# Performance work log

Hardware: AMD Instinct MI355X
Metric: run time of the kernel (lower is better)

Reference implementation:

```python
import jax, jax.numpy as jnp
import numpy as np
from jax import lax

B, T, C_IN, C_OUT, HW = 4, 8, 64, 64, 96

def conv2d(x, w, b):
    # x: [B,C,H,W], w: [O,I,3,3] (OIHW), SAME padding, stride 1
    y = lax.conv_general_dilated(x, w, (1, 1), 'SAME',
                                 dimension_numbers=('NCHW', 'OIHW', 'NCHW'))
    return y + b[None, :, None, None]

def setup_inputs() -> dict:
    key = jax.random.key(0)
    ks = jax.random.split(key, 4)
    s = 1.0 / np.sqrt((C_IN + C_OUT) * 9)
    return {
        'x': jax.random.normal(ks[0], (B, T, C_IN, HW, HW), jnp.float32),
        'w_r': jax.random.normal(ks[1], (C_OUT, C_IN + C_OUT, 3, 3), jnp.float32) * s,
        'b_r': jnp.zeros((C_OUT,), jnp.float32),
        'w_z': jax.random.normal(ks[2], (C_OUT, C_IN + C_OUT, 3, 3), jnp.float32) * s,
        'b_z': jnp.zeros((C_OUT,), jnp.float32),
        'w_h': jax.random.normal(ks[3], (C_OUT, C_IN + C_OUT, 3, 3), jnp.float32) * s,
        'b_h': jnp.zeros((C_OUT,), jnp.float32),
    }

def reference(x, w_r, b_r, w_z, b_z, w_h, b_h):
    # x: [B,T,C_in,H,W] -> time-major [T,B,C_in,H,W]
    xt = jnp.transpose(x.reshape(B, T, C_IN, HW, HW), (1, 0, 2, 3, 4))
    h0 = jnp.zeros((B, C_OUT, HW, HW), x.dtype)

    def step(h, x_i):
        xh = jnp.concatenate([x_i, h], axis=1)          # [B, C_in+C_out, H, W]
        r = jax.nn.sigmoid(conv2d(xh, w_r, b_r))         # reset gate
        z = jax.nn.sigmoid(conv2d(xh, w_z, b_z))         # update gate
        h_tilde = jnp.tanh(conv2d(jnp.concatenate([x_i, r * h], axis=1), w_h, b_h))
        h_new = (1.0 - z) * h + z * h_tilde
        return h_new, h_new

    _, outs = lax.scan(step, h0, xt)                     # [T,B,C_out,H,W]
    outs = jnp.transpose(outs, (1, 0, 2, 3, 4))          # [B,T,C_out,H,W]
    return outs.reshape(-1, C_OUT, HW, HW)               # [B*T,C_out,H,W]
```

## Files before the change

kernel.cpp:

```cpp
#include <hip/hip_runtime.h>
#include <hip/hip_fp16.h>

#define HWD  96
#define NPIX (HWD*HWD)
#define CIN  64
#define COUT 64
#define CTOT 128
#define BB   4
#define TT   8
#define WSTR (CTOT*9)

typedef short bf16x8 __attribute__((ext_vector_type(8)));
typedef float f32x4  __attribute__((ext_vector_type(4)));

__device__ __forceinline__ float sigmoid_(float v){ return 1.0f/(1.0f+__expf(-v)); }
__device__ __forceinline__ float tanh_(float v){
    float e = __expf(2.0f*fabsf(v));
    float t = 1.0f - 2.0f/(e+1.0f);
    return copysignf(t, v);
}
__device__ __forceinline__ short f2bf(float f){
    unsigned u = __float_as_uint(f);
    u += 0x7fffu + ((u>>16)&1u);
    return (short)(u>>16);
}
__device__ __forceinline__ short f2h(float f){
    return (short)__half_as_ushort(__float2half(f));
}
__device__ __forceinline__ float h2f(short s){
    return __half2float(__ushort_as_half((unsigned short)s));
}

__global__ __launch_bounds__(256) void convert_x_all(const float* __restrict__ x,
                                                     short* __restrict__ xt){
    __shared__ float tile[64][65];
    const int bt  = blockIdx.y;
    const int px0 = blockIdx.x * 64;
    const float* src = x + (size_t)bt*CIN*NPIX;
    short* dst = xt + (size_t)bt*NPIX*CIN;
    const int tid = threadIdx.x;
#pragma unroll
    for (int i = 0; i < 16; ++i){
        int ic = i*4 + (tid>>6);
        int pl = tid & 63;
        tile[ic][pl] = src[(size_t)ic*NPIX + px0 + pl];
    }
    __syncthreads();
#pragma unroll
    for (int i = 0; i < 16; ++i){
        int ic = tid & 63;
        int pl = i*4 + (tid>>6);
        dst[(size_t)(px0+pl)*CIN + ic] = f2bf(tile[ic][pl]);
    }
}

__global__ __launch_bounds__(256) void convert_x(const float* __restrict__ x,
                                                 short* __restrict__ xt, int t){
    __shared__ float tile[64][65];
    const int b   = blockIdx.y;
    const int px0 = blockIdx.x * 64;
    const float* src = x + ((size_t)(b*TT + t)*CIN)*NPIX;
    short* dst = xt + ((size_t)b*NPIX)*CIN;
    const int tid = threadIdx.x;
#pragma unroll
    for (int i = 0; i < 16; ++i){
        int ic = i*4 + (tid>>6);
        int pl = tid & 63;
        tile[ic][pl] = src[(size_t)ic*NPIX + px0 + pl];
    }
    __syncthreads();
#pragma unroll
    for (int i = 0; i < 16; ++i){
        int ic = tid & 63;
        int pl = i*4 + (tid>>6);
        dst[(size_t)(px0+pl)*CIN + ic] = f2bf(tile[ic][pl]);
    }
}

__global__ __launch_bounds__(256) void convert_w(const float* __restrict__ wr,
    const float* __restrict__ wz, const float* __restrict__ wh,
    short* __restrict__ wfrag, short* __restrict__ zpad){
    const int g = blockIdx.x*256 + threadIdx.x;
    if (g < 128) zpad[g] = 0;
    const int lane = g & 63, rest = g >> 6;
    const int mt = rest & 3, kc = (rest>>2)&3, rem = rest>>4;
    const int tap = rem % 9, c = rem / 9;
    const float* wsrc = (c==0) ? wr : (c==1) ? wz : wh;
    const int oc  = mt*16 + (lane&15);
    const int ctb = kc*32 + (lane>>4)*8;
    bf16x8 v;
#pragma unroll
    for (int j=0;j<8;++j)
        v[j] = f2bf(wsrc[(size_t)oc*WSTR + (size_t)(ctb+j)*9 + tap]);
    *(bf16x8*)(wfrag + (size_t)g*8) = v;
}

__global__ __launch_bounds__(256) void precompute_ux(
    const short* __restrict__ xt, const short* __restrict__ wfrag,
    const short* __restrict__ zpad, short* __restrict__ ux)
{
    const int lane = threadIdx.x & 63;
    const int wave = threadIdx.x >> 6;
    const int quad = lane >> 4, col = lane & 15;
    const int bt = blockIdx.y, c = blockIdx.z;
    const int n_base = blockIdx.x*128 + wave*32;

    int px[2], xx[2], yy[2];
#pragma unroll
    for (int nt=0; nt<2; ++nt){
        px[nt] = n_base + nt*16 + col;
        yy[nt] = px[nt]/HWD;
        xx[nt] = px[nt] - yy[nt]*HWD;
    }

    f32x4 acc[4][2];
#pragma unroll
    for (int mt=0;mt<4;++mt)
#pragma unroll
    for (int nt=0;nt<2;++nt) acc[mt][nt] = f32x4{0.f,0.f,0.f,0.f};

    const short* xs = xt + (size_t)bt*NPIX*CIN;
    for (int tap=0; tap<9; ++tap){
        const int ky = tap/3, kx = tap-3*ky;
        const int off = (ky-1)*HWD + (kx-1);
        const short* bp[2];
#pragma unroll
        for (int nt=0;nt<2;++nt){
            bool v = ((unsigned)(yy[nt]+ky-1) < HWD) && ((unsigned)(xx[nt]+kx-1) < HWD);
            bp[nt] = v ? (xs + (size_t)(px[nt]+off)*CIN) : zpad;
        }
#pragma unroll
        for (int kcl=0; kcl<2; ++kcl){
            bf16x8 bfr[2];
#pragma unroll
            for (int nt=0;nt<2;++nt)
                bfr[nt] = *(const bf16x8*)(bp[nt] + kcl*32 + quad*8);
            const short* wc = wfrag + (size_t)(((c*9+tap)*4 + kcl)*4)*64*8;
#pragma unroll
            for (int mt=0;mt<4;++mt){
                bf16x8 a = *(const bf16x8*)(wc + (size_t)(mt*64+lane)*8);
#pragma unroll
                for (int nt=0;nt<2;++nt)
                    acc[mt][nt] = __builtin_amdgcn_mfma_f32_16x16x32_bf16(
                        a, bfr[nt], acc[mt][nt], 0, 0, 0);
            }
        }
    }

    short* uxs = ux + ((size_t)c*(BB*TT) + bt)*NPIX*COUT;
#pragma unroll
    for (int mt=0; mt<4; ++mt){
        const int ocb = mt*16 + quad*4;
#pragma unroll
        for (int nt=0; nt<2; ++nt){
            short4 v;
            v.x = f2h(acc[mt][nt][0]); v.y = f2h(acc[mt][nt][1]);
            v.z = f2h(acc[mt][nt][2]); v.w = f2h(acc[mt][nt][3]);
            *(short4*)(uxs + (size_t)px[nt]*COUT + ocb) = v;
        }
    }
}

__global__ __launch_bounds__(256) void gates2(
    const short* __restrict__ htb, const short* __restrict__ wfrag,
    const short* __restrict__ zpad, const short* __restrict__ ux,
    const float* __restrict__ br, const float* __restrict__ bz,
    float* __restrict__ out, short* __restrict__ rht, int t)
{
    const int lane = threadIdx.x & 63;
    const int wave = threadIdx.x >> 6;
    const int quad = lane >> 4, col = lane & 15;
    const int b = blockIdx.y, c = blockIdx.z;
    const int n_base = blockIdx.x*128 + wave*32;

    int px[2], xx[2], yy[2];
#pragma unroll
    for (int nt=0; nt<2; ++nt){
        px[nt] = n_base + nt*16 + col;
        yy[nt] = px[nt]/HWD;
        xx[nt] = px[nt] - yy[nt]*HWD;
    }

    const short* uxs = ux + (((size_t)c*BB + b)*TT + t)*NPIX*COUT;
    short4 uxv[4][2];
#pragma unroll
    for (int mt=0; mt<4; ++mt)
#pragma unroll
    for (int nt=0; nt<2; ++nt)
        uxv[mt][nt] = *(const short4*)(uxs + (size_t)px[nt]*COUT + mt*16 + quad*4);

    f32x4 acc[4][2];
#pragma unroll
    for (int mt=0;mt<4;++mt)
#pragma unroll
    for (int nt=0;nt<2;++nt) acc[mt][nt] = f32x4{0.f,0.f,0.f,0.f};

    if (t > 0){
        const short* hs = htb + (size_t)b*NPIX*COUT;
        for (int tap=0; tap<9; ++tap){
            const int ky = tap/3, kx = tap-3*ky;
            const int off = (ky-1)*HWD + (kx-1);
            const short* bp[2];
#pragma unroll
            for (int nt=0;nt<2;++nt){
                bool v = ((unsigned)(yy[nt]+ky-1) < HWD) && ((unsigned)(xx[nt]+kx-1) < HWD);
                bp[nt] = v ? (hs + (size_t)(px[nt]+off)*COUT) : zpad;
            }
#pragma unroll
            for (int kcl=0; kcl<2; ++kcl){
                bf16x8 bfr[2];
#pragma unroll
                for (int nt=0;nt<2;++nt)
                    bfr[nt] = *(const bf16x8*)(bp[nt] + kcl*32 + quad*8);
                const short* wc = wfrag + (size_t)(((c*9+tap)*4 + 2+kcl)*4)*64*8;
#pragma unroll
                for (int mt=0;mt<4;++mt){
                    bf16x8 a = *(const bf16x8*)(wc + (size_t)(mt*64+lane)*8);
#pragma unroll
                    for (int nt=0;nt<2;++nt)
                        acc[mt][nt] = __builtin_amdgcn_mfma_f32_16x16x32_bf16(
                            a, bfr[nt], acc[mt][nt], 0, 0, 0);
                }
            }
        }
    }

    const float* hprev = out + ((size_t)(b*TT+t-1)*COUT)*NPIX;
    if (c == 0){
        short* rhs = rht + (size_t)b*NPIX*COUT;
#pragma unroll
        for (int mt=0; mt<4; ++mt){
            const int ocb = mt*16 + quad*4;
#pragma unroll
            for (int nt=0; nt<2; ++nt){
                const int p = px[nt];
                const short* uq = (const short*)&uxv[mt][nt];
                short rh4[4];
#pragma unroll
                for (int reg=0; reg<4; ++reg){
                    const int oc = ocb + reg;
                    float r  = sigmoid_(acc[mt][nt][reg] + h2f(uq[reg]) + br[oc]);
                    float hv = (t>0) ? hprev[(size_t)oc*NPIX + p] : 0.0f;
                    rh4[reg] = f2bf(r*hv);
                }
                *(short4*)(rhs + (size_t)p*COUT + ocb) =
                    make_short4(rh4[0], rh4[1], rh4[2], rh4[3]);
            }
        }
    } else {
        float* zout = out + ((size_t)(b*TT+t)*COUT)*NPIX;
#pragma unroll
        for (int mt=0; mt<4; ++mt){
            const int ocb = mt*16 + quad*4;
#pragma unroll
            for (int nt=0; nt<2; ++nt){
                const int p = px[nt];
                const short* uq = (const short*)&uxv[mt][nt];
#pragma unroll
                for (int reg=0; reg<4; ++reg){
                    const int oc = ocb + reg;
                    zout[(size_t)oc*NPIX + p] =
                        sigmoid_(acc[mt][nt][reg] + h2f(uq[reg]) + bz[oc]);
                }
            }
        }
    }
}

__global__ __launch_bounds__(256) void cand2(
    const short* __restrict__ rht, const short* __restrict__ wfrag,
    const short* __restrict__ zpad, const short* __restrict__ ux,
    const float* __restrict__ bh, float* __restrict__ out,
    short* __restrict__ htb, int t)
{
    const int lane = threadIdx.x & 63;
    const int wave = threadIdx.x >> 6;
    const int quad = lane >> 4, col = lane & 15;
    const int b = blockIdx.y, mh = blockIdx.z;
    const int n_base = blockIdx.x*128 + wave*32;

    int px[2], xx[2], yy[2];
#pragma unroll
    for (int nt=0; nt<2; ++nt){
        px[nt] = n_base + nt*16 + col;
        yy[nt] = px[nt]/HWD;
        xx[nt] = px[nt] - yy[nt]*HWD;
    }

    const short* uxs = ux + (((size_t)2*BB + b)*TT + t)*NPIX*COUT;
    short4 uxv[2][2];
#pragma unroll
    for (int mtl=0; mtl<2; ++mtl)
#pragma unroll
    for (int nt=0; nt<2; ++nt)
        uxv[mtl][nt] = *(const short4*)(uxs + (size_t)px[nt]*COUT + (mh*2+mtl)*16 + quad*4);

    f32x4 acc[2][2];
#pragma unroll
    for (int mtl=0;mtl<2;++mtl)
#pragma unroll
    for (int nt=0;nt<2;++nt) acc[mtl][nt] = f32x4{0.f,0.f,0.f,0.f};

    if (t > 0){
        const short* rs = rht + (size_t)b*NPIX*COUT;
        for (int tap=0; tap<9; ++tap){
            const int ky = tap/3, kx = tap-3*ky;
            const int off = (ky-1)*HWD + (kx-1);
            const short* bp[2];
#pragma unroll
            for (int nt=0;nt<2;++nt){
                bool v = ((unsigned)(yy[nt]+ky-1) < HWD) && ((unsigned)(xx[nt]+kx-1) < HWD);
                bp[nt] = v ? (rs + (size_t)(px[nt]+off)*COUT) : zpad;
            }
#pragma unroll
            for (int kcl=0; kcl<2; ++kcl){
                bf16x8 bfr[2];
#pragma unroll
                for (int nt=0;nt<2;++nt)
                    bfr[nt] = *(const bf16x8*)(bp[nt] + kcl*32 + quad*8);
                const short* wc = wfrag + (size_t)(((2*9+tap)*4 + 2+kcl)*4)*64*8;
#pragma unroll
                for (int mtl=0;mtl<2;++mtl){
                    const int mt = mh*2 + mtl;
                    bf16x8 a = *(const bf16x8*)(wc + (size_t)(mt*64+lane)*8);
#pragma unroll
                    for (int nt=0;nt<2;++nt)
                        acc[mtl][nt] = __builtin_amdgcn_mfma_f32_16x16x32_bf16(
                            a, bfr[nt], acc[mtl][nt], 0, 0, 0);
                }
            }
        }
    }

    float* o = out + ((size_t)(b*TT+t)*COUT)*NPIX;
    const float* hprev = out + ((size_t)(b*TT+t-1)*COUT)*NPIX;
    short* hts = htb + (size_t)b*NPIX*COUT;
#pragma unroll
    for (int mtl=0; mtl<2; ++mtl){
        const int ocb = (mh*2+mtl)*16 + quad*4;
#pragma unroll
        for (int nt=0; nt<2; ++nt){
            const int p = px[nt];
            const short* uq = (const short*)&uxv[mtl][nt];
            short h4[4];
#pragma unroll
            for (int reg=0; reg<4; ++reg){
                const int oc = ocb + reg;
                float htl = tanh_(acc[mtl][nt][reg] + h2f(uq[reg]) + bh[oc]);
                float z   = o[(size_t)oc*NPIX + p];
                float hv  = (t>0) ? hprev[(size_t)oc*NPIX + p] : 0.0f;
                float hn  = fmaf(z, htl - hv, hv);
                o[(size_t)oc*NPIX + p] = hn;
                h4[reg] = f2bf(hn);
            }
            *(short4*)(hts + (size_t)p*COUT + ocb) =
                make_short4(h4[0], h4[1], h4[2], h4[3]);
        }
    }
}

__global__ __launch_bounds__(256) void gates_mfma(
    const short* __restrict__ xt, const short* __restrict__ ht,
    const short* __restrict__ wfrag, const short* __restrict__ zpad,
    const float* __restrict__ br, const float* __restrict__ bz,
    float* __restrict__ out, short* __restrict__ rht, int t)
{
    const int lane = threadIdx.x & 63;
    const int wave = threadIdx.x >> 6;
    const int quad = lane >> 4, col = lane & 15;
    const int b = blockIdx.y;
    const int n_base = blockIdx.x*128 + wave*32;

    int px[2], xx[2], yy[2];
#pragma unroll
    for (int nt=0; nt<2; ++nt){
        px[nt] = n_base + nt*16 + col;
        yy[nt] = px[nt]/HWD;
        xx[nt] = px[nt] - yy[nt]*HWD;
    }
    f32x4 acc[2][4][2];
#pragma unroll
    for(int c=0;c<2;++c)
#pragma unroll
    for(int mt=0;mt<4;++mt)
#pragma unroll
    for(int nt=0;nt<2;++nt) acc[c][mt][nt] = f32x4{0.f,0.f,0.f,0.f};

    const short* xs = xt + ((size_t)b*NPIX)*CIN;
    const short* hs = ht + ((size_t)b*NPIX)*COUT;
    const int nparts = (t>0) ? 2 : 1;
    for (int part=0; part<nparts; ++part){
        const short* src = part ? hs : xs;
        for (int tap=0; tap<9; ++tap){
            const int ky = tap/3, kx = tap-3*ky;
            const int off = (ky-1)*HWD + (kx-1);
            const short* bp[2];
#pragma unroll
            for (int nt=0;nt<2;++nt){
                bool v = ((unsigned)(yy[nt]+ky-1) < HWD) && ((unsigned)(xx[nt]+kx-1) < HWD);
                bp[nt] = v ? (src + (size_t)(px[nt]+off)*CIN) : zpad;
            }
#pragma unroll
            for (int kcl=0; kcl<2; ++kcl){
                const int kc = part*2 + kcl;
                bf16x8 bfr[2];
#pragma unroll
                for (int nt=0;nt<2;++nt)
                    bfr[nt] = *(const bf16x8*)(bp[nt] + kcl*32 + quad*8);
#pragma unroll
                for (int c=0;c<2;++c){
                    const short* wc = wfrag + (size_t)(((c*9+tap)*4 + kc)*4)*64*8;
#pragma unroll
                    for (int mt=0;mt<4;++mt){
                        bf16x8 a = *(const bf16x8*)(wc + (size_t)(mt*64+lane)*8);
#pragma unroll
                        for (int nt=0;nt<2;++nt)
                            acc[c][mt][nt] = __builtin_amdgcn_mfma_f32_16x16x32_bf16(
                                a, bfr[nt], acc[c][mt][nt], 0, 0, 0);
                    }
                }
            }
        }
    }
    float* zout = out + ((size_t)(b*TT+t)*COUT)*NPIX;
    const float* hprev = out + ((size_t)(b*TT+t-1)*COUT)*NPIX;
    short* rhs = rht + ((size_t)b*NPIX)*COUT;
#pragma unroll
    for (int mt=0; mt<4; ++mt){
        const int ocb = mt*16 + quad*4;
#pragma unroll
        for (int nt=0; nt<2; ++nt){
            const int p = px[nt];
            short rh4[4];
#pragma unroll
            for (int reg=0; reg<4; ++reg){
                const int oc = ocb + reg;
                float z = sigmoid_(acc[1][mt][nt][reg] + bz[oc]);
                zout[(size_t)oc*NPIX + p] = z;
                float hv = (t>0) ? hprev[(size_t)oc*NPIX + p] : 0.0f;
                float r  = sigmoid_(acc[0][mt][nt][reg] + br[oc]);
                rh4[reg] = f2bf(r*hv);
            }
            *(short4*)(rhs + (size_t)p*COUT + ocb) =
                make_short4(rh4[0], rh4[1], rh4[2], rh4[3]);
        }
    }
}

__global__ __launch_bounds__(256) void cand_mfma(
    const short* __restrict__ xt, const short* __restrict__ rht,
    const short* __restrict__ wfrag, const short* __restrict__ zpad,
    const float* __restrict__ bh,
    float* __restrict__ out, short* __restrict__ ht, int t)
{
    const int lane = threadIdx.x & 63;
    const int wave = threadIdx.x >> 6;
    const int quad = lane >> 4, col = lane & 15;
    const int b = blockIdx.y;
    const int n_base = blockIdx.x*128 + wave*32;

    int px[2], xx[2], yy[2];
#pragma unroll
    for (int nt=0; nt<2; ++nt){
        px[nt] = n_base + nt*16 + col;
        yy[nt] = px[nt]/HWD;
        xx[nt] = px[nt] - yy[nt]*HWD;
    }
    f32x4 acc[4][2];
#pragma unroll
    for(int mt=0;mt<4;++mt)
#pragma unroll
    for(int nt=0;nt<2;++nt) acc[mt][nt] = f32x4{0.f,0.f,0.f,0.f};

    const short* xs = xt + ((size_t)b*NPIX)*CIN;
    const short* rs = rht + ((size_t)b*NPIX)*COUT;
    const int nparts = (t>0) ? 2 : 1;
    for (int part=0; part<nparts; ++part){
        const short* src = part ? rs : xs;
        for (int tap=0; tap<9; ++tap){
            const int ky = tap/3, kx = tap-3*ky;
            const int off = (ky-1)*HWD + (kx-1);
            const short* bp[2];
#pragma unroll
            for (int nt=0;nt<2;++nt){
                bool v = ((unsigned)(yy[nt]+ky-1) < HWD) && ((unsigned)(xx[nt]+kx-1) < HWD);
                bp[nt] = v ? (src + (size_t)(px[nt]+off)*CIN) : zpad;
            }
#pragma unroll
            for (int kcl=0; kcl<2; ++kcl){
                const int kc = part*2 + kcl;
                bf16x8 bfr[2];
#pragma unroll
                for (int nt=0;nt<2;++nt)
                    bfr[nt] = *(const bf16x8*)(bp[nt] + kcl*32 + quad*8);
                const short* wc = wfrag + (size_t)(((2*9+tap)*4 + kc)*4)*64*8;
#pragma unroll
                for (int mt=0;mt<4;++mt){
                    bf16x8 a = *(const bf16x8*)(wc + (size_t)(mt*64+lane)*8);
#pragma unroll
                    for (int nt=0;nt<2;++nt)
                        acc[mt][nt] = __builtin_amdgcn_mfma_f32_16x16x32_bf16(
                            a, bfr[nt], acc[mt][nt], 0, 0, 0);
                }
            }
        }
    }
    float* o = out + ((size_t)(b*TT+t)*COUT)*NPIX;
    const float* hprev = out + ((size_t)(b*TT+t-1)*COUT)*NPIX;
    short* hts = ht + ((size_t)b*NPIX)*COUT;
#pragma unroll
    for (int mt=0; mt<4; ++mt){
        const int ocb = mt*16 + quad*4;
#pragma unroll
        for (int nt=0; nt<2; ++nt){
            const int p = px[nt];
            short h4[4];
#pragma unroll
            for (int reg=0; reg<4; ++reg){
                const int oc = ocb + reg;
                float htl = tanh_(acc[mt][nt][reg] + bh[oc]);
                float z   = o[(size_t)oc*NPIX + p];
                float hv  = (t>0) ? hprev[(size_t)oc*NPIX + p] : 0.0f;
                float hn  = fmaf(z, htl - hv, hv);
                o[(size_t)oc*NPIX + p] = hn;
                h4[reg] = f2bf(hn);
            }
            *(short4*)(hts + (size_t)p*COUT + ocb) =
                make_short4(h4[0], h4[1], h4[2], h4[3]);
        }
    }
}

extern "C" void kernel_launch(void* const* d_in, const int* in_sizes, int n_in,
                              void* d_out, int out_size, void* d_ws, size_t ws_size,
                              hipStream_t stream) {
    const float* x  = (const float*)d_in[0];
    const float* wr = (const float*)d_in[1];
    const float* br = (const float*)d_in[2];
    const float* wz = (const float*)d_in[3];
    const float* bz = (const float*)d_in[4];
    const float* wh = (const float*)d_in[5];
    const float* bh = (const float*)d_in[6];
    float* out = (float*)d_out;

    const size_t nxt_all = (size_t)BB*TT*NPIX*CIN;
    const size_t nh      = (size_t)BB*NPIX*COUT;
    const size_t nwf     = (size_t)3*9*4*4*64*8;
    const size_t nux     = (size_t)3*BB*TT*NPIX*COUT;
    const size_t need    = (nxt_all + 2*nh + nwf + 128 + nux) * sizeof(short);

    if (ws_size >= need) {
        short* xt  = (short*)d_ws;
        short* htb = xt  + nxt_all;
        short* rht = htb + nh;
        short* wf  = rht + nh;
        short* zp  = wf  + nwf;
        short* ux  = zp  + 128;

        convert_w<<<108, 256, 0, stream>>>(wr, wz, wh, wf, zp);
        convert_x_all<<<dim3(NPIX/64, BB*TT), 256, 0, stream>>>(x, xt);
        precompute_ux<<<dim3(NPIX/128, BB*TT, 3), 256, 0, stream>>>(xt, wf, zp, ux);
        for (int t = 0; t < TT; ++t) {
            gates2<<<dim3(NPIX/128, BB, 2), 256, 0, stream>>>(htb, wf, zp, ux, br, bz, out, rht, t);
            cand2 <<<dim3(NPIX/128, BB, 2), 256, 0, stream>>>(rht, wf, zp, ux, bh, out, htb, t);
        }
    } else {
        short* xt  = (short*)d_ws;
        short* htb = xt  + (size_t)BB*NPIX*CIN;
        short* rht = htb + nh;
        short* wf  = rht + nh;
        short* zp  = wf  + nwf;
        convert_w<<<108, 256, 0, stream>>>(wr, wz, wh, wf, zp);
        dim3 cxgrid(NPIX/64, BB);
        dim3 ggrid(NPIX/128, BB);
        for (int t = 0; t < TT; ++t) {
            convert_x<<<cxgrid, 256, 0, stream>>>(x, xt, t);
            gates_mfma<<<ggrid, 256, 0, stream>>>(xt, htb, wf, zp, br, bz, out, rht, t);
            cand_mfma <<<ggrid, 256, 0, stream>>>(xt, rht, wf, zp, bh, out, htb, t);
        }
    }
}
```

Baseline: 716.3 us.

## Stage recurrent state in LDS with halo and reshape input-conv precompute

The recurrent gate and candidate kernels now load a 128-pixel tile plus a one-row halo of the bf16 hidden state (or r*h) into shared memory once, then read all nine conv taps from LDS instead of global memory. Blocks grow to 512 threads with one 16-pixel column per wave. The reset path also reads h from the staged bf16 tile instead of the fp32 output. The input-conv precompute now has each block compute all three gates for half the output channels, so the x fragments loaded are reused across gates. The cost is about 46 KB of LDS per block, which limits occupancy, plus an extra barrier, and r*h now uses a bf16-rounded h.

```diff
diff --git a/kernel.cpp b/kernel.cpp
--- a/kernel.cpp
+++ b/kernel.cpp
@@ -10,6 +10,11 @@
 #define TT   8
 #define WSTR (CTOT*9)
 
+#define TILE 128
+#define HALO 97
+#define SPX  (TILE + 2*HALO)
+#define LROW 72
+
 typedef short bf16x8 __attribute__((ext_vector_type(8)));
 typedef float f32x4  __attribute__((ext_vector_type(4)));
 
@@ -23,6 +28,9 @@
     unsigned u = __float_as_uint(f);
     u += 0x7fffu + ((u>>16)&1u);
     return (short)(u>>16);
+}
+__device__ __forceinline__ float b2f(short s){
+    return __uint_as_float(((unsigned)(unsigned short)s) << 16);
 }
 __device__ __forceinline__ short f2h(float f){
     return (short)__half_as_ushort(__float2half(f));
@@ -95,14 +103,14 @@
     *(bf16x8*)(wfrag + (size_t)g*8) = v;
 }
 
-__global__ __launch_bounds__(256) void precompute_ux(
+__global__ __launch_bounds__(256) void precompute_ux3(
     const short* __restrict__ xt, const short* __restrict__ wfrag,
     const short* __restrict__ zpad, short* __restrict__ ux)
 {
     const int lane = threadIdx.x & 63;
     const int wave = threadIdx.x >> 6;
     const int quad = lane >> 4, col = lane & 15;
-    const int bt = blockIdx.y, c = blockIdx.z;
+    const int bt = blockIdx.y, mh = blockIdx.z;
     const int n_base = blockIdx.x*128 + wave*32;
 
     int px[2], xx[2], yy[2];
@@ -113,11 +121,13 @@
         xx[nt] = px[nt] - yy[nt]*HWD;
     }
 
-    f32x4 acc[4][2];
-#pragma unroll
-    for (int mt=0;mt<4;++mt)
-#pragma unroll
-    for (int nt=0;nt<2;++nt) acc[mt][nt] = f32x4{0.f,0.f,0.f,0.f};
+    f32x4 acc[3][2][2];
+#pragma unroll
+    for (int c=0;c<3;++c)
+#pragma unroll
+    for (int mtl=0;mtl<2;++mtl)
+#pragma unroll
+    for (int nt=0;nt<2;++nt) acc[c][mtl][nt] = f32x4{0.f,0.f,0.f,0.f};
 
     const short* xs = xt + (size_t)bt*NPIX*CIN;
     for (int tap=0; tap<9; ++tap){
@@ -135,198 +145,193 @@
 #pragma unroll
             for (int nt=0;nt<2;++nt)
                 bfr[nt] = *(const bf16x8*)(bp[nt] + kcl*32 + quad*8);
-            const short* wc = wfrag + (size_t)(((c*9+tap)*4 + kcl)*4)*64*8;
-#pragma unroll
-            for (int mt=0;mt<4;++mt){
-                bf16x8 a = *(const bf16x8*)(wc + (size_t)(mt*64+lane)*8);
-#pragma unroll
-                for (int nt=0;nt<2;++nt)
-                    acc[mt][nt] = __builtin_amdgcn_mfma_f32_16x16x32_bf16(
-                        a, bfr[nt], acc[mt][nt], 0, 0, 0);
-            }
-        }
-    }
-
-    short* uxs = ux + ((size_t)c*(BB*TT) + bt)*NPIX*COUT;
-#pragma unroll
-    for (int mt=0; mt<4; ++mt){
-        const int ocb = mt*16 + quad*4;
-#pragma unroll
-        for (int nt=0; nt<2; ++nt){
-            short4 v;
-            v.x = f2h(acc[mt][nt][0]); v.y = f2h(acc[mt][nt][1]);
-            v.z = f2h(acc[mt][nt][2]); v.w = f2h(acc[mt][nt][3]);
-            *(short4*)(uxs + (size_t)px[nt]*COUT + ocb) = v;
-        }
-    }
-}
-
-__global__ __launch_bounds__(256) void gates2(
+#pragma unroll
+            for (int c=0;c<3;++c){
+                const short* wc = wfrag + (size_t)(((c*9+tap)*4 + kcl)*4)*64*8;
+#pragma unroll
+                for (int mtl=0;mtl<2;++mtl){
+                    const int mt = mh*2 + mtl;
+                    bf16x8 a = *(const bf16x8*)(wc + (size_t)(mt*64+lane)*8);
+#pragma unroll
+                    for (int nt=0;nt<2;++nt)
+                        acc[c][mtl][nt] = __builtin_amdgcn_mfma_f32_16x16x32_bf16(
+                            a, bfr[nt], acc[c][mtl][nt], 0, 0, 0);
+                }
+            }
+        }
+    }
+
+#pragma unroll
+    for (int c=0;c<3;++c){
+        short* uxs = ux + ((size_t)c*(BB*TT) + bt)*NPIX*COUT;
+#pragma unroll
+        for (int mtl=0; mtl<2; ++mtl){
+            const int ocb = (mh*2+mtl)*16 + quad*4;
+#pragma unroll
+            for (int nt=0; nt<2; ++nt){
+                short4 v;
+                v.x = f2h(acc[c][mtl][nt][0]); v.y = f2h(acc[c][mtl][nt][1]);
+                v.z = f2h(acc[c][mtl][nt][2]); v.w = f2h(acc[c][mtl][nt][3]);
+                *(short4*)(uxs + (size_t)px[nt]*COUT + ocb) = v;
+            }
+        }
+    }
+}
+
+__global__ __launch_bounds__(512) void gates3(
     const short* __restrict__ htb, const short* __restrict__ wfrag,
-    const short* __restrict__ zpad, const short* __restrict__ ux,
+    const short* __restrict__ ux,
     const float* __restrict__ br, const float* __restrict__ bz,
     float* __restrict__ out, short* __restrict__ rht, int t)
 {
-    const int lane = threadIdx.x & 63;
-    const int wave = threadIdx.x >> 6;
+    __shared__ short hls[SPX*LROW];
+    const int tid = threadIdx.x;
+    const int lane = tid & 63, wave = tid >> 6;
     const int quad = lane >> 4, col = lane & 15;
     const int b = blockIdx.y, c = blockIdx.z;
-    const int n_base = blockIdx.x*128 + wave*32;
-
-    int px[2], xx[2], yy[2];
-#pragma unroll
-    for (int nt=0; nt<2; ++nt){
-        px[nt] = n_base + nt*16 + col;
-        yy[nt] = px[nt]/HWD;
-        xx[nt] = px[nt] - yy[nt]*HWD;
-    }
-
-    const short* uxs = ux + (((size_t)c*BB + b)*TT + t)*NPIX*COUT;
-    short4 uxv[4][2];
-#pragma unroll
-    for (int mt=0; mt<4; ++mt)
-#pragma unroll
-    for (int nt=0; nt<2; ++nt)
-        uxv[mt][nt] = *(const short4*)(uxs + (size_t)px[nt]*COUT + mt*16 + quad*4);
-
-    f32x4 acc[4][2];
-#pragma unroll
-    for (int mt=0;mt<4;++mt)
-#pragma unroll
-    for (int nt=0;nt<2;++nt) acc[mt][nt] = f32x4{0.f,0.f,0.f,0.f};
+    const int p0 = blockIdx.x*TILE;
+    const int px = p0 + wave*16 + col;
+    const int yy = px/HWD, xx = px - yy*HWD;
+    const int lpc = px - (p0 - HALO);
 
     if (t > 0){
         const short* hs = htb + (size_t)b*NPIX*COUT;
+        const int p_lo = p0 - HALO;
+#pragma unroll
+        for (int r = 0; r < 6; ++r){
+            int e = r*512 + tid;
+            if (e < SPX*8){
+                int lp = e >> 3, ck = (e & 7) * 8;
+                int gp = min(max(p_lo + lp, 0), NPIX-1);
+                *(int4*)&hls[lp*LROW + ck] = *(const int4*)&hs[(size_t)gp*COUT + ck];
+            }
+        }
+    }
+
+    const short* uxs = ux + (((size_t)c*BB + b)*TT + t)*NPIX*COUT;
+    short4 uxv[4];
+#pragma unroll
+    for (int mt=0; mt<4; ++mt)
+        uxv[mt] = *(const short4*)(uxs + (size_t)px*COUT + mt*16 + quad*4);
+
+    f32x4 acc[4];
+#pragma unroll
+    for (int mt=0;mt<4;++mt) acc[mt] = f32x4{0.f,0.f,0.f,0.f};
+
+    if (t > 0){
+        __syncthreads();
+        const bf16x8 zv = {};
         for (int tap=0; tap<9; ++tap){
             const int ky = tap/3, kx = tap-3*ky;
             const int off = (ky-1)*HWD + (kx-1);
-            const short* bp[2];
-#pragma unroll
-            for (int nt=0;nt<2;++nt){
-                bool v = ((unsigned)(yy[nt]+ky-1) < HWD) && ((unsigned)(xx[nt]+kx-1) < HWD);
-                bp[nt] = v ? (hs + (size_t)(px[nt]+off)*COUT) : zpad;
-            }
+            const bool v = ((unsigned)(yy+ky-1) < HWD) && ((unsigned)(xx+kx-1) < HWD);
+            const short* bbase = &hls[(lpc + off)*LROW];
 #pragma unroll
             for (int kcl=0; kcl<2; ++kcl){
-                bf16x8 bfr[2];
-#pragma unroll
-                for (int nt=0;nt<2;++nt)
-                    bfr[nt] = *(const bf16x8*)(bp[nt] + kcl*32 + quad*8);
+                bf16x8 bfr = *(const bf16x8*)(bbase + kcl*32 + quad*8);
+                bfr = v ? bfr : zv;
                 const short* wc = wfrag + (size_t)(((c*9+tap)*4 + 2+kcl)*4)*64*8;
 #pragma unroll
                 for (int mt=0;mt<4;++mt){
                     bf16x8 a = *(const bf16x8*)(wc + (size_t)(mt*64+lane)*8);
-#pragma unroll
-                    for (int nt=0;nt<2;++nt)
-                        acc[mt][nt] = __builtin_amdgcn_mfma_f32_16x16x32_bf16(
-                            a, bfr[nt], acc[mt][nt], 0, 0, 0);
+                    acc[mt] = __builtin_amdgcn_mfma_f32_16x16x32_bf16(a, bfr, acc[mt], 0, 0, 0);
                 }
             }
         }
     }
 
-    const float* hprev = out + ((size_t)(b*TT+t-1)*COUT)*NPIX;
     if (c == 0){
         short* rhs = rht + (size_t)b*NPIX*COUT;
 #pragma unroll
         for (int mt=0; mt<4; ++mt){
             const int ocb = mt*16 + quad*4;
-#pragma unroll
-            for (int nt=0; nt<2; ++nt){
-                const int p = px[nt];
-                const short* uq = (const short*)&uxv[mt][nt];
-                short rh4[4];
-#pragma unroll
-                for (int reg=0; reg<4; ++reg){
-                    const int oc = ocb + reg;
-                    float r  = sigmoid_(acc[mt][nt][reg] + h2f(uq[reg]) + br[oc]);
-                    float hv = (t>0) ? hprev[(size_t)oc*NPIX + p] : 0.0f;
-                    rh4[reg] = f2bf(r*hv);
-                }
-                *(short4*)(rhs + (size_t)p*COUT + ocb) =
-                    make_short4(rh4[0], rh4[1], rh4[2], rh4[3]);
-            }
+            short4 h4 = make_short4(0,0,0,0);
+            if (t > 0) h4 = *(const short4*)&hls[lpc*LROW + ocb];
+            const short* uq = (const short*)&uxv[mt];
+            const short* hq = (const short*)&h4;
+            short rh4[4];
+#pragma unroll
+            for (int reg=0; reg<4; ++reg){
+                const int oc = ocb + reg;
+                float r = sigmoid_(acc[mt][reg] + h2f(uq[reg]) + br[oc]);
+                rh4[reg] = f2bf(r * b2f(hq[reg]));
+            }
+            *(short4*)(rhs + (size_t)px*COUT + ocb) =
+                make_short4(rh4[0], rh4[1], rh4[2], rh4[3]);
         }
     } else {
         float* zout = out + ((size_t)(b*TT+t)*COUT)*NPIX;
 #pragma unroll
         for (int mt=0; mt<4; ++mt){
             const int ocb = mt*16 + quad*4;
-#pragma unroll
-            for (int nt=0; nt<2; ++nt){
-                const int p = px[nt];
-                const short* uq = (const short*)&uxv[mt][nt];
-#pragma unroll
-                for (int reg=0; reg<4; ++reg){
-                    const int oc = ocb + reg;
-                    zout[(size_t)oc*NPIX + p] =
-                        sigmoid_(acc[mt][nt][reg] + h2f(uq[reg]) + bz[oc]);
-                }
-            }
-        }
-    }
-}
-
-__global__ __launch_bounds__(256) void cand2(
+            const short* uq = (const short*)&uxv[mt];
+#pragma unroll
+            for (int reg=0; reg<4; ++reg){
+                const int oc = ocb + reg;
+                zout[(size_t)oc*NPIX + px] =
+                    sigmoid_(acc[mt][reg] + h2f(uq[reg]) + bz[oc]);
+            }
+        }
+    }
+}
+
+__global__ __launch_bounds__(512) void cand3(
     const short* __restrict__ rht, const short* __restrict__ wfrag,
-    const short* __restrict__ zpad, const short* __restrict__ ux,
-    const float* __restrict__ bh, float* __restrict__ out,
-    short* __restrict__ htb, int t)
+    const short* __restrict__ ux, const float* __restrict__ bh,
+    float* __restrict__ out, short* __restrict__ htb, int t)
 {
-    const int lane = threadIdx.x & 63;
-    const int wave = threadIdx.x >> 6;
+    __shared__ short rls[SPX*LROW];
+    const int tid = threadIdx.x;
+    const int lane = tid & 63, wave = tid >> 6;
     const int quad = lane >> 4, col = lane & 15;
     const int b = blockIdx.y, mh = blockIdx.z;
-    const int n_base = blockIdx.x*128 + wave*32;
-
-    int px[2], xx[2], yy[2];
-#pragma unroll
-    for (int nt=0; nt<2; ++nt){
-        px[nt] = n_base + nt*16 + col;
-        yy[nt] = px[nt]/HWD;
-        xx[nt] = px[nt] - yy[nt]*HWD;
-    }
-
-    const short* uxs = ux + (((size_t)2*BB + b)*TT + t)*NPIX*COUT;
-    short4 uxv[2][2];
-#pragma unroll
-    for (int mtl=0; mtl<2; ++mtl)
-#pragma unroll
-    for (int nt=0; nt<2; ++nt)
-        uxv[mtl][nt] = *(const short4*)(uxs + (size_t)px[nt]*COUT + (mh*2+mtl)*16 + quad*4);
-
-    f32x4 acc[2][2];
-#pragma unroll
-    for (int mtl=0;mtl<2;++mtl)
-#pragma unroll
-    for (int nt=0;nt<2;++nt) acc[mtl][nt] = f32x4{0.f,0.f,0.f,0.f};
+    const int p0 = blockIdx.x*TILE;
+    const int px = p0 + wave*16 + col;
+    const int yy = px/HWD, xx = px - yy*HWD;
+    const int lpc = px - (p0 - HALO);
 
     if (t > 0){
         const short* rs = rht + (size_t)b*NPIX*COUT;
+        const int p_lo = p0 - HALO;
+#pragma unroll
+        for (int r = 0; r < 6; ++r){
+            int e = r*512 + tid;
+            if (e < SPX*8){
+                int lp = e >> 3, ck = (e & 7) * 8;
+                int gp = min(max(p_lo + lp, 0), NPIX-1);
+                *(int4*)&rls[lp*LROW + ck] = *(const int4*)&rs[(size_t)gp*COUT + ck];
+            }
+        }
+    }
+
+    const short* uxs = ux + (((size_t)2*BB + b)*TT + t)*NPIX*COUT;
+    short4 uxv[2];
+#pragma unroll
+    for (int mtl=0; mtl<2; ++mtl)
+        uxv[mtl] = *(const short4*)(uxs + (size_t)px*COUT + (mh*2+mtl)*16 + quad*4);
+
+    f32x4 acc[2];
+#pragma unroll
+    for (int mtl=0;mtl<2;++mtl) acc[mtl] = f32x4{0.f,0.f,0.f,0.f};
+
+    if (t > 0){
+        __syncthreads();
+        const bf16x8 zv = {};
         for (int tap=0; tap<9; ++tap){
             const int ky = tap/3, kx = tap-3*ky;
             const int off = (ky-1)*HWD + (kx-1);
-            const short* bp[2];
-#pragma unroll
-            for (int nt=0;nt<2;++nt){
-                bool v = ((unsigned)(yy[nt]+ky-1) < HWD) && ((unsigned)(xx[nt]+kx-1) < HWD);
-                bp[nt] = v ? (rs + (size_t)(px[nt]+off)*COUT) : zpad;
-            }
+            const bool v = ((unsigned)(yy+ky-1) < HWD) && ((unsigned)(xx+kx-1) < HWD);
+            const short* bbase = &rls[(lpc + off)*LROW];
 #pragma unroll
             for (int kcl=0; kcl<2; ++kcl){
-                bf16x8 bfr[2];
-#pragma unroll
-                for (int nt=0;nt<2;++nt)
-                    bfr[nt] = *(const bf16x8*)(bp[nt] + kcl*32 + quad*8);
+                bf16x8 bfr = *(const bf16x8*)(bbase + kcl*32 + quad*8);
+                bfr = v ? bfr : zv;
                 const short* wc = wfrag + (size_t)(((2*9+tap)*4 + 2+kcl)*4)*64*8;
 #pragma unroll
                 for (int mtl=0;mtl<2;++mtl){
                     const int mt = mh*2 + mtl;
                     bf16x8 a = *(const bf16x8*)(wc + (size_t)(mt*64+lane)*8);
-#pragma unroll
-                    for (int nt=0;nt<2;++nt)
-                        acc[mtl][nt] = __builtin_amdgcn_mfma_f32_16x16x32_bf16(
-                            a, bfr[nt], acc[mtl][nt], 0, 0, 0);
+                    acc[mtl] = __builtin_amdgcn_mfma_f32_16x16x32_bf16(a, bfr, acc[mtl], 0, 0, 0);
                 }
             }
         }
@@ -338,24 +343,20 @@
 #pragma unroll
     for (int mtl=0; mtl<2; ++mtl){
         const int ocb = (mh*2+mtl)*16 + quad*4;
-#pragma unroll
-        for (int nt=0; nt<2; ++nt){
-            const int p = px[nt];
-            const short* uq = (const short*)&uxv[mtl][nt];
-            short h4[4];
-#pragma unroll
-            for (int reg=0; reg<4; ++reg){
-                const int oc = ocb + reg;
-                float htl = tanh_(acc[mtl][nt][reg] + h2f(uq[reg]) + bh[oc]);
-                float z   = o[(size_t)oc*NPIX + p];
-                float hv  = (t>0) ? hprev[(size_t)oc*NPIX + p] : 0.0f;
-                float hn  = fmaf(z, htl - hv, hv);
-                o[(size_t)oc*NPIX + p] = hn;
-                h4[reg] = f2bf(hn);
-            }
-            *(short4*)(hts + (size_t)p*COUT + ocb) =
-                make_short4(h4[0], h4[1], h4[2], h4[3]);
-        }
+        const short* uq = (const short*)&uxv[mtl];
+        short h4[4];
+#pragma unroll
+        for (int reg=0; reg<4; ++reg){
+            const int oc = ocb + reg;
+            float htl = tanh_(acc[mtl][reg] + h2f(uq[reg]) + bh[oc]);
+            float z   = o[(size_t)oc*NPIX + px];
+            float hv  = (t>0) ? hprev[(size_t)oc*NPIX + px] : 0.0f;
+            float hn  = fmaf(z, htl - hv, hv);
+            o[(size_t)oc*NPIX + px] = hn;
+            h4[reg] = f2bf(hn);
+        }
+        *(short4*)(hts + (size_t)px*COUT + ocb) =
+            make_short4(h4[0], h4[1], h4[2], h4[3]);
     }
 }
 
@@ -559,10 +560,10 @@
 
         convert_w<<<108, 256, 0, stream>>>(wr, wz, wh, wf, zp);
         convert_x_all<<<dim3(NPIX/64, BB*TT), 256, 0, stream>>>(x, xt);
-        precompute_ux<<<dim3(NPIX/128, BB*TT, 3), 256, 0, stream>>>(xt, wf, zp, ux);
+        precompute_ux3<<<dim3(NPIX/128, BB*TT, 2), 256, 0, stream>>>(xt, wf, zp, ux);
         for (int t = 0; t < TT; ++t) {
-            gates2<<<dim3(NPIX/128, BB, 2), 256, 0, stream>>>(htb, wf, zp, ux, br, bz, out, rht, t);
-            cand2 <<<dim3(NPIX/128, BB, 2), 256, 0, stream>>>(rht, wf, zp, ux, bh, out, htb, t);
+            gates3<<<dim3(NPIX/TILE, BB, 2), 512, 0, stream>>>(htb, wf, ux, br, bz, out, rht, t);
+            cand3 <<<dim3(NPIX/TILE, BB, 2), 512, 0, stream>>>(rht, wf, ux, bh, out, htb, t);
         }
     } else {
         short* xt  = (short*)d_ws;
```

After: 601.2 us. 1.19x faster.
